# Optimization experiments

Measured on AMD Instinct MI355X. Metric: run time of the kernel, lower is better.

## Reference

```python
import jax, jax.numpy as jnp
import numpy as np

CLAMP_MAX = float(np.log(100.0))  # temperature clamp from MoELayer


def setup_inputs() -> dict:
    key = jax.random.key(0)
    ks = jax.random.split(key, 4)
    N, D, H, E = 524288, 128, 512, 8
    x = jax.random.normal(ks[0], (N, D), dtype=jnp.float32)
    # per-expert MLP params, stacked along expert axis; scaled like torch Linear init
    W1 = jax.random.normal(ks[1], (E, D, H), dtype=jnp.float32) / np.sqrt(D)
    b1 = jnp.zeros((E, H), dtype=jnp.float32)
    W2 = jax.random.normal(ks[2], (E, H, D), dtype=jnp.float32) / np.sqrt(H)
    b2 = jnp.zeros((E, D), dtype=jnp.float32)
    temperature = jnp.full((1,), np.log(2.0), dtype=jnp.float32)  # init from MoELayer
    return {"x": x, "W1": W1, "b1": b1, "W2": W2, "b2": b2,
            "temperature": temperature}


def reference(x, W1, b1, W2, b2, temperature):
    # Pretraining proportional router: tokens split into E contiguous equal
    # chunks (route_prob == 1), so dispatch/combine is a reshape.
    E = W1.shape[0]
    N, D = x.shape
    xe = x.reshape(E, N // E, D)                      # [E, n, D] dispatched tokens
    h = jax.nn.relu(jnp.einsum('end,edh->enh', xe, W1) + b1[:, None, :])
    y = jnp.einsum('enh,ehd->end', h, W2) + b2[:, None, :]
    logit_scale = jnp.exp(jnp.minimum(temperature, CLAMP_MAX))  # scalar [1]
    out = y.reshape(N, D) * logit_scale
    return out
```

## Files before the change

### kernel.cpp

```cpp
#include <hip/hip_runtime.h>


#define CLAMP_MAXV 4.605170185988091f

typedef __attribute__((ext_vector_type(8))) short s16x8;
typedef __attribute__((ext_vector_type(4))) float f32x4;
typedef __attribute__((ext_vector_type(4))) unsigned short u16x4;
typedef __attribute__((ext_vector_type(8))) unsigned short u16x8;

static __device__ __forceinline__ unsigned short f2bf(float f) {
  union { float f; unsigned int u; } v; v.f = f;
  unsigned int r = v.u + 0x7FFFu + ((v.u >> 16) & 1u);
  return (unsigned short)(r >> 16);
}

static __device__ __forceinline__ void gll16(const void* src, void* dst) {
  __builtin_amdgcn_global_load_lds((const __attribute__((address_space(1))) void*)src,
                                   (__attribute__((address_space(3))) void*)dst, 16, 0, 0);
}

#define LBAR() do { \
  asm volatile("s_waitcnt lgkmcnt(0)" ::: "memory"); \
  __builtin_amdgcn_s_barrier(); \
  __builtin_amdgcn_sched_barrier(0); \
} while (0)

__global__ void conv_w(const float* __restrict__ W1, const float* __restrict__ W2,
                       unsigned short* __restrict__ w1t, unsigned short* __restrict__ w2t) {
  int idx = blockIdx.x * 256 + threadIdx.x;
  if (idx < 65536) {
    int h  = idx & 511;
    int d0 = ((idx >> 9) & 15) << 3;
    int e  = idx >> 13;
    const float* src = W1 + ((size_t)e << 16);
    u16x8 v;
#pragma unroll
    for (int j = 0; j < 8; ++j) v[j] = f2bf(src[(size_t)(d0 + j) * 512 + h]);
    *(u16x8*)(w1t + ((((size_t)e << 9) + h) << 7) + d0) = v;
  } else {
    int i2 = idx - 65536;
    int d  = i2 & 127;
    int h0 = ((i2 >> 7) & 63) << 3;
    int e  = i2 >> 13;
    const float* src = W2 + ((size_t)e << 16);
    u16x8 v;
#pragma unroll
    for (int j = 0; j < 8; ++j) v[j] = f2bf(src[(size_t)(h0 + j) * 128 + d]);
    *(u16x8*)(w2t + ((((size_t)e << 7) + d) << 9) + h0) = v;
  }
}

__global__ __launch_bounds__(1024, 4) void moe_fused(
    const float* __restrict__ x,
    const float* __restrict__ b1,
    const float* __restrict__ b2,
    const float* __restrict__ temp,
    const unsigned short* __restrict__ w1t,
    const unsigned short* __restrict__ w2t,
    float* __restrict__ out)
{
  __shared__ __align__(16) char smem[133120];
  char* const w1s  = smem;
  char* const hsb0 = smem + 98304;
  char* const hsb1 = smem + 106496;
  char* const xs   = smem + 114688;
  float* const b1s = (float*)(smem + 131072);

  const int tid  = threadIdx.x;
  const int lane = tid & 63;
  const int wid  = tid >> 6;
  const int l15  = lane & 15;
  const int lg   = lane >> 4;
  const int blk  = blockIdx.x;
  const int e    = blk >> 6;
  const size_t tok0 = (size_t)blk << 10;

  const unsigned short* w1g = w1t + ((size_t)e << 16);
  const unsigned short* w2g = w2t + ((size_t)e << 16);
  const float* xblk = x + (tok0 << 7);
  float* const oblk = out + (tok0 << 7);

#pragma unroll
  for (int k = 0; k < 6; ++k) {
    int s = tid + (k << 10);
    int hl = s >> 4, sr = s & 15;
    gll16(w1g + ((size_t)(hl + 128) << 7) + ((sr ^ (hl & 7)) << 3), w1s + (s << 4));
  }

  if (tid < 512) b1s[tid] = b1[(e << 9) + tid];

  f32x4 xv[2];
  xv[0] = *(const f32x4*)(xblk + (tid << 3));
  xv[1] = *(const f32x4*)(xblk + (tid << 3) + 4);

  const int xtok = tid >> 4;
  const unsigned xaddr = (unsigned)((xtok << 8) + ((tid & 15) << 4)) ^ (unsigned)((xtok & 7) << 4);

  if (wid < 8) {
    const int hr  = wid & 3;
    const int tq0 = (wid >> 2) << 5;
    const unsigned hl2 = (unsigned)(((hr << 4) + (lg << 2)) << 1);

    s16x8 w1r[2][4];
#pragma unroll
    for (int c = 0; c < 2; ++c) {
      const int hrow = (c << 6) + (hr << 4) + l15;
#pragma unroll
      for (int ks = 0; ks < 4; ++ks)
        w1r[c][ks] = *(const s16x8*)(w1g + ((size_t)hrow << 7) + (ks << 5) + (lg << 3));
    }

    __syncthreads();

#pragma unroll 1
    for (int t = 0; t < 16; ++t) {
      u16x8 p;
#pragma unroll
      for (int i = 0; i < 8; ++i) p[i] = f2bf(xv[i >> 2][i & 3]);
      *(u16x8*)(xs + xaddr) = p;
      LBAR();

      s16x8 xb[2][4];
#pragma unroll
      for (int j = 0; j < 2; ++j) {
        int tk = tq0 + (j << 4) + l15;
#pragma unroll
        for (int ks = 0; ks < 4; ++ks) {
          unsigned koff = (unsigned)((ks << 6) + (lg << 4));
          xb[j][ks] = *(const s16x8*)(xs + (((unsigned)(tk << 8) + koff) ^ (unsigned)((tk & 7) << 4)));
        }
      }

#pragma unroll
      for (int c = 0; c <= 8; ++c) {
        if (c < 8) {
          f32x4 bias = *(const f32x4*)(b1s + (c << 6) + (hr << 4) + (lg << 2));
          f32x4 acc1[2];
          acc1[0] = (f32x4){0.f, 0.f, 0.f, 0.f};
          acc1[1] = (f32x4){0.f, 0.f, 0.f, 0.f};
          if (c < 2) {
#pragma unroll
            for (int j = 0; j < 2; ++j)
#pragma unroll
              for (int ks = 0; ks < 4; ++ks)
                acc1[j] = __builtin_amdgcn_mfma_f32_16x16x32_bf16(w1r[c][ks], xb[j][ks], acc1[j], 0, 0, 0);
          } else {
            const int hrow = (c << 6) + (hr << 4) + l15;
            const unsigned hswz = (unsigned)((hrow & 7) << 4);
            s16x8 a[4];
#pragma unroll
            for (int ks = 0; ks < 4; ++ks) {
              unsigned koff = (unsigned)((ks << 6) + (lg << 4));
              a[ks] = *(const s16x8*)(w1s + (((unsigned)((hrow - 128) << 8) + koff) ^ hswz));
            }
#pragma unroll
            for (int j = 0; j < 2; ++j)
#pragma unroll
              for (int ks = 0; ks < 4; ++ks)
                acc1[j] = __builtin_amdgcn_mfma_f32_16x16x32_bf16(a[ks], xb[j][ks], acc1[j], 0, 0, 0);
          }

          char* const hw = (c & 1) ? hsb1 : hsb0;
#pragma unroll
          for (int j = 0; j < 2; ++j) {
            int tk = tq0 + (j << 4) + l15;
            u16x4 qv;
#pragma unroll
            for (int r = 0; r < 4; ++r)
              qv[r] = f2bf(fmaxf(acc1[j][r] + bias[r], 0.f));
            *(u16x4*)(hw + (((unsigned)(tk << 7) + hl2) ^ (unsigned)((tk & 7) << 4))) = qv;
          }
        }
        if (c == 4 && t < 15) {
          const float* xn = xblk + (((size_t)t + 1) << 13);
          xv[0] = *(const f32x4*)(xn + (tid << 3));
          xv[1] = *(const f32x4*)(xn + (tid << 3) + 4);
        }
        LBAR();
      }
    }
  } else {
    const int cw = wid - 8;
    const int dlane = (cw << 4) + l15;

    s16x8 w2f[8][2];
#pragma unroll
    for (int c = 0; c < 8; ++c)
#pragma unroll
      for (int ks = 0; ks < 2; ++ks)
        w2f[c][ks] = *(const s16x8*)(w2g + ((size_t)dlane << 9) + (c << 6) + (ks << 5) + (lg << 3));

    const float b2v   = b2[(e << 7) + dlane];
    const float scale = expf(fminf(temp[0], CLAMP_MAXV));

    __syncthreads();

#pragma unroll 1
    for (int t = 0; t < 16; ++t) {
      u16x8 p;
#pragma unroll
      for (int i = 0; i < 8; ++i) p[i] = f2bf(xv[i >> 2][i & 3]);
      *(u16x8*)(xs + xaddr) = p;
      LBAR();

      f32x4 acc2[4];
#pragma unroll
      for (int i = 0; i < 4; ++i) acc2[i] = (f32x4){0.f, 0.f, 0.f, 0.f};

#pragma unroll
      for (int c = 0; c <= 8; ++c) {
        if (c >= 1) {
          const int cc = c - 1;
          char* const hrd = (cc & 1) ? hsb1 : hsb0;
#pragma unroll
          for (int ii = 0; ii < 4; ++ii) {
            int tk = (ii << 4) + l15;
            unsigned tswz = (unsigned)((tk & 7) << 4);
#pragma unroll
            for (int ks = 0; ks < 2; ++ks) {
              unsigned koff = (unsigned)((ks << 6) + (lg << 4));
              s16x8 ha = *(const s16x8*)(hrd + (((unsigned)(tk << 7) + koff) ^ tswz));
              acc2[ii] = __builtin_amdgcn_mfma_f32_16x16x32_bf16(ha, w2f[cc][ks], acc2[ii], 0, 0, 0);
            }
          }
        }
        if (c == 4 && t < 15) {
          const float* xn = xblk + (((size_t)t + 1) << 13);
          xv[0] = *(const f32x4*)(xn + (tid << 3));
          xv[1] = *(const f32x4*)(xn + (tid << 3) + 4);
        }
        LBAR();
      }

      float* og = oblk + ((size_t)t << 13);
#pragma unroll
      for (int i = 0; i < 4; ++i) {
#pragma unroll
        for (int r = 0; r < 4; ++r) {
          int tk = (i << 4) + (lg << 2) + r;
          og[((size_t)tk << 7) + dlane] = (acc2[i][r] + b2v) * scale;
        }
      }
    }
  }
}

__global__ void moe_naive(const float* __restrict__ x, const float* __restrict__ W1,
                          const float* __restrict__ b1, const float* __restrict__ W2,
                          const float* __restrict__ b2, const float* __restrict__ temp,
                          float* __restrict__ out) {
  __shared__ float xr[128];
  __shared__ float hrow[512];
  int t = blockIdx.x;
  int e = t >> 16;
  int tx = threadIdx.x;
  xr[tx] = x[((size_t)t << 7) + tx];
  __syncthreads();
  const float* w1e = W1 + ((size_t)e << 16);
  for (int h = tx; h < 512; h += 128) {
    float s = b1[(e << 9) + h];
    for (int d = 0; d < 128; ++d) s += xr[d] * w1e[(size_t)d * 512 + h];
    hrow[h] = fmaxf(s, 0.f);
  }
  __syncthreads();
  const float* w2e = W2 + ((size_t)e << 16);
  float s = b2[(e << 7) + tx];
  for (int h = 0; h < 512; ++h) s += hrow[h] * w2e[(size_t)h * 128 + tx];
  out[((size_t)t << 7) + tx] = s * expf(fminf(temp[0], CLAMP_MAXV));
}

extern "C" void kernel_launch(void* const* d_in, const int* in_sizes, int n_in,
                              void* d_out, int out_size, void* d_ws, size_t ws_size,
                              hipStream_t stream) {
  const float* x    = (const float*)d_in[0];
  const float* W1   = (const float*)d_in[1];
  const float* b1   = (const float*)d_in[2];
  const float* W2   = (const float*)d_in[3];
  const float* b2   = (const float*)d_in[4];
  const float* temp = (const float*)d_in[5];
  float* out = (float*)d_out;

  const size_t WS_NEEDED = 2u * 524288u * sizeof(unsigned short);
  if (ws_size >= WS_NEEDED) {
    unsigned short* w1t = (unsigned short*)d_ws;
    unsigned short* w2t = w1t + 524288;
    conv_w<<<512, 256, 0, stream>>>(W1, W2, w1t, w2t);
    moe_fused<<<512, 1024, 0, stream>>>(x, b1, b2, temp, w1t, w2t, out);
  } else {
    moe_naive<<<524288, 128, 0, stream>>>(x, W1, b1, W2, b2, temp, out);
  }
}
```

Baseline: 178.6 us.

## Stream W2 fragments per chunk and retile consumer waves to 2x2 output tiles

Measured after the change: 288.4 us. 61.5% more time.

```diff
diff --git a/kernel.cpp b/kernel.cpp
--- a/kernel.cpp
+++ b/kernel.cpp
@@ -181,19 +181,20 @@
     }
   } else {
     const int cw = wid - 8;
-    const int dlane = (cw << 4) + l15;
-
-    s16x8 w2f[8][2];
-#pragma unroll
-    for (int c = 0; c < 8; ++c)
-#pragma unroll
-      for (int ks = 0; ks < 2; ++ks)
-        w2f[c][ks] = *(const s16x8*)(w2g + ((size_t)dlane << 9) + (c << 6) + (ks << 5) + (lg << 3));
-
-    const float b2v   = b2[(e << 7) + dlane];
+    const int th = cw >> 2;
+    const int dq = cw & 3;
+    const int d0 = (dq << 5) + l15;
+
+    const float b2v0  = b2[(e << 7) + d0];
+    const float b2v1  = b2[(e << 7) + d0 + 16];
     const float scale = expf(fminf(temp[0], CLAMP_MAXV));
 
+    const unsigned short* w2base0 = w2g + ((size_t)d0 << 9) + (lg << 3);
+    const unsigned short* w2base1 = w2g + ((size_t)(d0 + 16) << 9) + (lg << 3);
+
     __syncthreads();
+
+    s16x8 w2s0[2][2], w2s1[2][2];
 
 #pragma unroll 1
     for (int t = 0; t < 16; ++t) {
@@ -203,24 +204,45 @@
       *(u16x8*)(xs + xaddr) = p;
       LBAR();
 
-      f32x4 acc2[4];
-#pragma unroll
-      for (int i = 0; i < 4; ++i) acc2[i] = (f32x4){0.f, 0.f, 0.f, 0.f};
+      f32x4 acc2[2][2];
+#pragma unroll
+      for (int ii = 0; ii < 2; ++ii)
+#pragma unroll
+        for (int j = 0; j < 2; ++j) acc2[ii][j] = (f32x4){0.f, 0.f, 0.f, 0.f};
 
 #pragma unroll
       for (int c = 0; c <= 8; ++c) {
+        if (c < 8) {
+          const int sl = c & 1;
+#pragma unroll
+          for (int ks = 0; ks < 2; ++ks) {
+            if (sl == 0) {
+              w2s0[0][ks] = *(const s16x8*)(w2base0 + (c << 6) + (ks << 5));
+              w2s1[0][ks] = *(const s16x8*)(w2base1 + (c << 6) + (ks << 5));
+            } else {
+              w2s0[1][ks] = *(const s16x8*)(w2base0 + (c << 6) + (ks << 5));
+              w2s1[1][ks] = *(const s16x8*)(w2base1 + (c << 6) + (ks << 5));
+            }
+          }
+        }
         if (c >= 1) {
           const int cc = c - 1;
           char* const hrd = (cc & 1) ? hsb1 : hsb0;
 #pragma unroll
-          for (int ii = 0; ii < 4; ++ii) {
-            int tk = (ii << 4) + l15;
+          for (int ii = 0; ii < 2; ++ii) {
+            int tk = (th << 5) + (ii << 4) + l15;
             unsigned tswz = (unsigned)((tk & 7) << 4);
 #pragma unroll
             for (int ks = 0; ks < 2; ++ks) {
               unsigned koff = (unsigned)((ks << 6) + (lg << 4));
               s16x8 ha = *(const s16x8*)(hrd + (((unsigned)(tk << 7) + koff) ^ tswz));
-              acc2[ii] = __builtin_amdgcn_mfma_f32_16x16x32_bf16(ha, w2f[cc][ks], acc2[ii], 0, 0, 0);
+              if ((cc & 1) == 0) {
+                acc2[ii][0] = __builtin_amdgcn_mfma_f32_16x16x32_bf16(ha, w2s0[0][ks], acc2[ii][0], 0, 0, 0);
+                acc2[ii][1] = __builtin_amdgcn_mfma_f32_16x16x32_bf16(ha, w2s1[0][ks], acc2[ii][1], 0, 0, 0);
+              } else {
+                acc2[ii][0] = __builtin_amdgcn_mfma_f32_16x16x32_bf16(ha, w2s0[1][ks], acc2[ii][0], 0, 0, 0);
+                acc2[ii][1] = __builtin_amdgcn_mfma_f32_16x16x32_bf16(ha, w2s1[1][ks], acc2[ii][1], 0, 0, 0);
+              }
             }
           }
         }
@@ -234,11 +256,12 @@
 
       float* og = oblk + ((size_t)t << 13);
 #pragma unroll
-      for (int i = 0; i < 4; ++i) {
+      for (int ii = 0; ii < 2; ++ii) {
 #pragma unroll
         for (int r = 0; r < 4; ++r) {
-          int tk = (i << 4) + (lg << 2) + r;
-          og[((size_t)tk << 7) + dlane] = (acc2[i][r] + b2v) * scale;
+          int tk = (th << 5) + (ii << 4) + (lg << 2) + r;
+          og[((size_t)tk << 7) + d0]      = (acc2[ii][0][r] + b2v0) * scale;
+          og[((size_t)tk << 7) + d0 + 16] = (acc2[ii][1][r] + b2v1) * scale;
         }
       }
     }
```

## Stream W1 chunks through double-buffered LDS instead of keeping them resident

Applied to the files above, without the earlier changes.

New measurement: 214.7 us. 1.2x slower.

```diff
diff --git a/kernel.cpp b/kernel.cpp
--- a/kernel.cpp
+++ b/kernel.cpp
@@ -18,12 +18,6 @@
   __builtin_amdgcn_global_load_lds((const __attribute__((address_space(1))) void*)src,
                                    (__attribute__((address_space(3))) void*)dst, 16, 0, 0);
 }
-
-#define LBAR() do { \
-  asm volatile("s_waitcnt lgkmcnt(0)" ::: "memory"); \
-  __builtin_amdgcn_s_barrier(); \
-  __builtin_amdgcn_sched_barrier(0); \
-} while (0)
 
 __global__ void conv_w(const float* __restrict__ W1, const float* __restrict__ W2,
                        unsigned short* __restrict__ w1t, unsigned short* __restrict__ w2t) {
@@ -50,6 +44,13 @@
   }
 }
 
+static __device__ __forceinline__ void stage_w1_chunk(
+    const unsigned short* __restrict__ w1g, char* dst, int cn, int tid) {
+  int hl = tid >> 4, sr = tid & 15;
+  gll16(w1g + ((size_t)((cn << 6) + hl) << 7) + ((sr ^ (hl & 7)) << 3),
+        dst + (tid << 4));
+}
+
 __global__ __launch_bounds__(1024, 4) void moe_fused(
     const float* __restrict__ x,
     const float* __restrict__ b1,
@@ -59,12 +60,13 @@
     const unsigned short* __restrict__ w2t,
     float* __restrict__ out)
 {
-  __shared__ __align__(16) char smem[133120];
-  char* const w1s  = smem;
-  char* const hsb0 = smem + 98304;
-  char* const hsb1 = smem + 106496;
-  char* const xs   = smem + 114688;
-  float* const b1s = (float*)(smem + 131072);
+  __shared__ __align__(16) char smem[67584];
+  char* const w1b0 = smem;
+  char* const w1b1 = smem + 16384;
+  char* const hsb0 = smem + 32768;
+  char* const hsb1 = smem + 40960;
+  char* const xs   = smem + 49152;
+  float* const b1s = (float*)(smem + 65536);
 
   const int tid  = threadIdx.x;
   const int lane = tid & 63;
@@ -80,13 +82,7 @@
   const float* xblk = x + (tok0 << 7);
   float* const oblk = out + (tok0 << 7);
 
-#pragma unroll
-  for (int k = 0; k < 6; ++k) {
-    int s = tid + (k << 10);
-    int hl = s >> 4, sr = s & 15;
-    gll16(w1g + ((size_t)(hl + 128) << 7) + ((sr ^ (hl & 7)) << 3), w1s + (s << 4));
-  }
-
+  stage_w1_chunk(w1g, w1b0, 0, tid);
   if (tid < 512) b1s[tid] = b1[(e << 9) + tid];
 
   f32x4 xv[2];
@@ -100,15 +96,8 @@
     const int hr  = wid & 3;
     const int tq0 = (wid >> 2) << 5;
     const unsigned hl2 = (unsigned)(((hr << 4) + (lg << 2)) << 1);
-
-    s16x8 w1r[2][4];
-#pragma unroll
-    for (int c = 0; c < 2; ++c) {
-      const int hrow = (c << 6) + (hr << 4) + l15;
-#pragma unroll
-      for (int ks = 0; ks < 4; ++ks)
-        w1r[c][ks] = *(const s16x8*)(w1g + ((size_t)hrow << 7) + (ks << 5) + (lg << 3));
-    }
+    const int hrl = (hr << 4) + l15;
+    const unsigned hswz = (unsigned)((hrl & 7) << 4);
 
     __syncthreads();
 
@@ -118,7 +107,7 @@
 #pragma unroll
       for (int i = 0; i < 8; ++i) p[i] = f2bf(xv[i >> 2][i & 3]);
       *(u16x8*)(xs + xaddr) = p;
-      LBAR();
+      __syncthreads();
 
       s16x8 xb[2][4];
 #pragma unroll
@@ -134,31 +123,24 @@
 #pragma unroll
       for (int c = 0; c <= 8; ++c) {
         if (c < 8) {
+          stage_w1_chunk(w1g, ((c + 1) & 1) ? w1b1 : w1b0, (c + 1) & 7, tid);
+
+          char* const wcur = (c & 1) ? w1b1 : w1b0;
+          s16x8 a[4];
+#pragma unroll
+          for (int ks = 0; ks < 4; ++ks) {
+            unsigned koff = (unsigned)((ks << 6) + (lg << 4));
+            a[ks] = *(const s16x8*)(wcur + (((unsigned)(hrl << 8) + koff) ^ hswz));
+          }
           f32x4 bias = *(const f32x4*)(b1s + (c << 6) + (hr << 4) + (lg << 2));
           f32x4 acc1[2];
           acc1[0] = (f32x4){0.f, 0.f, 0.f, 0.f};
           acc1[1] = (f32x4){0.f, 0.f, 0.f, 0.f};
-          if (c < 2) {
-#pragma unroll
-            for (int j = 0; j < 2; ++j)
-#pragma unroll
-              for (int ks = 0; ks < 4; ++ks)
-                acc1[j] = __builtin_amdgcn_mfma_f32_16x16x32_bf16(w1r[c][ks], xb[j][ks], acc1[j], 0, 0, 0);
-          } else {
-            const int hrow = (c << 6) + (hr << 4) + l15;
-            const unsigned hswz = (unsigned)((hrow & 7) << 4);
-            s16x8 a[4];
-#pragma unroll
-            for (int ks = 0; ks < 4; ++ks) {
-              unsigned koff = (unsigned)((ks << 6) + (lg << 4));
-              a[ks] = *(const s16x8*)(w1s + (((unsigned)((hrow - 128) << 8) + koff) ^ hswz));
-            }
-#pragma unroll
-            for (int j = 0; j < 2; ++j)
-#pragma unroll
-              for (int ks = 0; ks < 4; ++ks)
-                acc1[j] = __builtin_amdgcn_mfma_f32_16x16x32_bf16(a[ks], xb[j][ks], acc1[j], 0, 0, 0);
-          }
+#pragma unroll
+          for (int j = 0; j < 2; ++j)
+#pragma unroll
+            for (int ks = 0; ks < 4; ++ks)
+              acc1[j] = __builtin_amdgcn_mfma_f32_16x16x32_bf16(a[ks], xb[j][ks], acc1[j], 0, 0, 0);
 
           char* const hw = (c & 1) ? hsb1 : hsb0;
 #pragma unroll
@@ -176,7 +158,7 @@
           xv[0] = *(const f32x4*)(xn + (tid << 3));
           xv[1] = *(const f32x4*)(xn + (tid << 3) + 4);
         }
-        LBAR();
+        __syncthreads();
       }
     }
   } else {
@@ -201,7 +183,7 @@
 #pragma unroll
       for (int i = 0; i < 8; ++i) p[i] = f2bf(xv[i >> 2][i & 3]);
       *(u16x8*)(xs + xaddr) = p;
-      LBAR();
+      __syncthreads();
 
       f32x4 acc2[4];
 #pragma unroll
@@ -209,6 +191,9 @@
 
 #pragma unroll
       for (int c = 0; c <= 8; ++c) {
+        if (c < 8) {
+          stage_w1_chunk(w1g, ((c + 1) & 1) ? w1b1 : w1b0, (c + 1) & 7, tid);
+        }
         if (c >= 1) {
           const int cc = c - 1;
           char* const hrd = (cc & 1) ? hsb1 : hsb0;
@@ -229,7 +214,7 @@
           xv[0] = *(const f32x4*)(xn + (tid << 3));
           xv[1] = *(const f32x4*)(xn + (tid << 3) + 4);
         }
-        LBAR();
+        __syncthreads();
       }
 
       float* og = oblk + ((size_t)t << 13);
```

## Split consumer-wave K dimension with LDS reduction to reuse each H fragment across two MFMAs

Applied to the files above, without the earlier changes.

New measurement: 285.4 us. 1.6x slower.

```diff
diff --git a/kernel.cpp b/kernel.cpp
--- a/kernel.cpp
+++ b/kernel.cpp
@@ -64,6 +64,7 @@
   char* const hsb0 = smem + 98304;
   char* const hsb1 = smem + 106496;
   char* const xs   = smem + 114688;
+  char* const red  = smem + 98304;
   float* const b1s = (float*)(smem + 131072);
 
   const int tid  = threadIdx.x;
@@ -178,19 +179,26 @@
         }
         LBAR();
       }
+
+      LBAR();
+      LBAR();
     }
   } else {
     const int cw = wid - 8;
-    const int dlane = (cw << 4) + l15;
+    const int dq = cw & 3;
+    const int kh = cw >> 2;
+    char* const redq = red + (dq << 13);
 
     s16x8 w2f[8][2];
 #pragma unroll
     for (int c = 0; c < 8; ++c)
 #pragma unroll
-      for (int ks = 0; ks < 2; ++ks)
-        w2f[c][ks] = *(const s16x8*)(w2g + ((size_t)dlane << 9) + (c << 6) + (ks << 5) + (lg << 3));
-
-    const float b2v   = b2[(e << 7) + dlane];
+      for (int j = 0; j < 2; ++j)
+        w2f[c][j] = *(const s16x8*)(w2g + ((size_t)((dq << 5) + (j << 4) + l15) << 9)
+                                        + (c << 6) + (kh << 5) + (lg << 3));
+
+    const float b2v0  = b2[(e << 7) + (dq << 5) + l15];
+    const float b2v1  = b2[(e << 7) + (dq << 5) + 16 + l15];
     const float scale = expf(fminf(temp[0], CLAMP_MAXV));
 
     __syncthreads();
@@ -203,25 +211,26 @@
       *(u16x8*)(xs + xaddr) = p;
       LBAR();
 
-      f32x4 acc2[4];
-#pragma unroll
-      for (int i = 0; i < 4; ++i) acc2[i] = (f32x4){0.f, 0.f, 0.f, 0.f};
+      f32x4 acc2[4][2];
+#pragma unroll
+      for (int ii = 0; ii < 4; ++ii)
+#pragma unroll
+        for (int j = 0; j < 2; ++j) acc2[ii][j] = (f32x4){0.f, 0.f, 0.f, 0.f};
 
 #pragma unroll
       for (int c = 0; c <= 8; ++c) {
         if (c >= 1) {
           const int cc = c - 1;
           char* const hrd = (cc & 1) ? hsb1 : hsb0;
+          const unsigned koff = (unsigned)((kh << 6) + (lg << 4));
 #pragma unroll
           for (int ii = 0; ii < 4; ++ii) {
             int tk = (ii << 4) + l15;
             unsigned tswz = (unsigned)((tk & 7) << 4);
-#pragma unroll
-            for (int ks = 0; ks < 2; ++ks) {
-              unsigned koff = (unsigned)((ks << 6) + (lg << 4));
-              s16x8 ha = *(const s16x8*)(hrd + (((unsigned)(tk << 7) + koff) ^ tswz));
-              acc2[ii] = __builtin_amdgcn_mfma_f32_16x16x32_bf16(ha, w2f[cc][ks], acc2[ii], 0, 0, 0);
-            }
+            s16x8 ha = *(const s16x8*)(hrd + (((unsigned)(tk << 7) + koff) ^ tswz));
+#pragma unroll
+            for (int j = 0; j < 2; ++j)
+              acc2[ii][j] = __builtin_amdgcn_mfma_f32_16x16x32_bf16(ha, w2f[cc][j], acc2[ii][j], 0, 0, 0);
           }
         }
         if (c == 4 && t < 15) {
@@ -232,15 +241,42 @@
         LBAR();
       }
 
-      float* og = oblk + ((size_t)t << 13);
-#pragma unroll
-      for (int i = 0; i < 4; ++i) {
-#pragma unroll
-        for (int r = 0; r < 4; ++r) {
-          int tk = (i << 4) + (lg << 2) + r;
-          og[((size_t)tk << 7) + dlane] = (acc2[i][r] + b2v) * scale;
-        }
-      }
+      if (kh == 1) {
+#pragma unroll
+        for (int ii = 0; ii < 4; ++ii)
+#pragma unroll
+          for (int j = 0; j < 2; ++j) {
+            int dl = (j << 4) + l15;
+            unsigned addr = (unsigned)((dl << 8) + (((ii << 4) + (lg << 2)) << 2))
+                          ^ (unsigned)((dl & 7) << 4);
+            *(f32x4*)(redq + addr) = acc2[ii][j];
+          }
+      }
+      LBAR();
+      if (kh == 0) {
+#pragma unroll
+        for (int ii = 0; ii < 4; ++ii)
+#pragma unroll
+          for (int j = 0; j < 2; ++j) {
+            int dl = (j << 4) + l15;
+            unsigned addr = (unsigned)((dl << 8) + (((ii << 4) + (lg << 2)) << 2))
+                          ^ (unsigned)((dl & 7) << 4);
+            f32x4 v = *(const f32x4*)(redq + addr);
+            acc2[ii][j][0] += v[0]; acc2[ii][j][1] += v[1];
+            acc2[ii][j][2] += v[2]; acc2[ii][j][3] += v[3];
+          }
+        float* og = oblk + ((size_t)t << 13);
+#pragma unroll
+        for (int ii = 0; ii < 4; ++ii) {
+#pragma unroll
+          for (int r = 0; r < 4; ++r) {
+            int tk = (ii << 4) + (lg << 2) + r;
+            og[((size_t)tk << 7) + (dq << 5) + l15]      = (acc2[ii][0][r] + b2v0) * scale;
+            og[((size_t)tk << 7) + (dq << 5) + 16 + l15] = (acc2[ii][1][r] + b2v1) * scale;
+          }
+        }
+      }
+      LBAR();
     }
   }
 }
```
